# Kernel tuning notes

Hardware: AMD Instinct MI355X
Metric: run time of the kernel (lower is better)

Reference implementation:

```python
import jax, jax.numpy as jnp
import numpy as np

NUM_LAYERS = 25
INPUT = 500
HIDDEN = 64
SEQ = 25
BATCH = 4096
OUT = 10
GATES = 4 * HIDDEN


def setup_inputs() -> dict:
    key = jax.random.key(0)
    ks = jax.random.split(key, 11)
    s = 0.1  # ~ uniform(-1/sqrt(H),1/sqrt(H)) scale used by torch LSTM init
    return {
        "x": jax.random.normal(ks[0], (SEQ, BATCH, INPUT), jnp.float32),
        "W_ih0": jax.random.normal(ks[1], (GATES, INPUT), jnp.float32) * s,
        "W_hh0": jax.random.normal(ks[2], (GATES, HIDDEN), jnp.float32) * s,
        "b_ih0": jax.random.normal(ks[3], (GATES,), jnp.float32) * s,
        "b_hh0": jax.random.normal(ks[4], (GATES,), jnp.float32) * s,
        "W_ih_rest": jax.random.normal(ks[5], (NUM_LAYERS - 1, GATES, HIDDEN), jnp.float32) * s,
        "W_hh_rest": jax.random.normal(ks[6], (NUM_LAYERS - 1, GATES, HIDDEN), jnp.float32) * s,
        "b_ih_rest": jax.random.normal(ks[7], (NUM_LAYERS - 1, GATES), jnp.float32) * s,
        "b_hh_rest": jax.random.normal(ks[8], (NUM_LAYERS - 1, GATES), jnp.float32) * s,
        "W_lin": jax.random.normal(ks[9], (OUT, HIDDEN), jnp.float32) * s,
        "b_lin": jax.random.normal(ks[10], (OUT,), jnp.float32) * s,
    }


def _lstm_layer(seq, Wih, Whh, bih, bhh):
    # seq: [T, B, D_in] -> (outputs [T, B, H], h_T [B, H], c_T [B, H])
    T, B, _ = seq.shape
    H = Whh.shape[1]
    # precompute input projection for all timesteps in one big GEMM
    xp = jnp.einsum('tbi,gi->tbg', seq, Wih) + bih + bhh  # [T, B, 4H]
    h0 = jnp.zeros((B, H), seq.dtype)
    c0 = jnp.zeros((B, H), seq.dtype)

    def step(carry, xpt):
        h, c = carry
        g = xpt + h @ Whh.T  # [B, 4H], torch gate order i, f, g, o
        i, f, gg, o = jnp.split(g, 4, axis=-1)
        c = jax.nn.sigmoid(f) * c + jax.nn.sigmoid(i) * jnp.tanh(gg)
        h = jax.nn.sigmoid(o) * jnp.tanh(c)
        return (h, c), h

    (hT, cT), hs = jax.lax.scan(step, (h0, c0), xp)
    return hs, hT, cT


def reference(x, W_ih0, W_hh0, b_ih0, b_hh0, W_ih_rest, W_hh_rest, b_ih_rest, b_hh_rest, W_lin, b_lin):
    hs, hT, cT = _lstm_layer(x, W_ih0, W_hh0, b_ih0, b_hh0)
    h_list, c_list = [hT], [cT]
    for l in range(NUM_LAYERS - 1):  # fixed small layer count: Python loop ok
        hs, hT, cT = _lstm_layer(hs, W_ih_rest[l], W_hh_rest[l], b_ih_rest[l], b_hh_rest[l])
        h_list.append(hT)
        c_list.append(cT)
    h_n = jnp.stack(h_list)  # [L, B, H]
    c_n = jnp.stack(c_list)  # [L, B, H]
    # faithful to torch: out[:, -1, :] indexes the BATCH dim -> [T, H]
    lstm_out = hs[:, -1, :] @ W_lin.T + b_lin  # [T, OUT]
    return (lstm_out, h_n, c_n)
```

## Files before the change

kernel.cpp:

```cpp
#include <hip/hip_runtime.h>

#define T_SEQ 25
#define NBATCH 4096
#define D_IN 500
#define HID 64
#define NG 256
#define NLAYERS 25
#define NOUT 10

typedef __attribute__((ext_vector_type(8))) short bf16x8;
typedef __attribute__((ext_vector_type(4))) short bf16x4;
typedef __attribute__((ext_vector_type(4))) float f32x4;

#define LOG2E 1.4426950408889634f
#define ROWS 1152
#define RNG_OFF 57600

__device__ __forceinline__ short f2bf(float f) {
    union { float f; unsigned u; } v; v.f = f;
    unsigned u = v.u + 0x7FFFu + ((v.u >> 16) & 1u);
    return (short)(u >> 16);
}
__device__ __forceinline__ float bf2f(short s) {
    union { unsigned u; float f; } v;
    v.u = ((unsigned)(unsigned short)s) << 16;
    return v.f;
}
__device__ __forceinline__ bf16x8 cvt8(f32x4 a, f32x4 b) {
    bf16x8 r;
    r[0]=f2bf(a[0]); r[1]=f2bf(a[1]); r[2]=f2bf(a[2]); r[3]=f2bf(a[3]);
    r[4]=f2bf(b[0]); r[5]=f2bf(b[1]); r[6]=f2bf(b[2]); r[7]=f2bf(b[3]);
    return r;
}

__global__ __launch_bounds__(256)
void prep(const float* __restrict__ Wih0, const float* __restrict__ Whh0,
          const float* __restrict__ WihR, const float* __restrict__ WhhR,
          const float* __restrict__ bihR, const float* __restrict__ bhhR,
          short* __restrict__ wbf2, short* __restrict__ whh0b,
          short* __restrict__ wihRb, short* __restrict__ whhRb,
          float* __restrict__ bsum) {
    int idx = blockIdx.x * 256 + threadIdx.x;
    if (idx < 131072) {
        int j = idx & 7, lane = (idx >> 3) & 63, nt = (idx >> 9) & 15, kc = idx >> 13;
        int n = nt*16 + (lane & 15);
        int k = kc*32 + (lane >> 4)*8 + j;
        wbf2[idx] = (k < D_IN) ? f2bf(Wih0[n * D_IN + k]) : (short)0;
    } else if (idx < 147456) {
        int j = idx - 131072; whh0b[j] = f2bf(Whh0[j]);
    } else if (idx < 540672) {
        int j = idx - 147456; wihRb[j] = f2bf(WihR[j]);
    } else if (idx < 933888) {
        int j = idx - 540672; whhRb[j] = f2bf(WhhR[j]);
    } else if (idx < 940032) {
        int j = idx - 933888; bsum[j] = bihR[j] + bhhR[j];
    }
}

__global__ __launch_bounds__(256, 1)
void xp0_gemm(const float* __restrict__ x, const short* __restrict__ wbf2,
              const float* __restrict__ bih0, const float* __restrict__ bhh0,
              short* __restrict__ xp0b) {
    const int tid = threadIdx.x;
    const int wv = tid >> 6, lane = tid & 63, col = lane & 15, q = lane >> 4;
    const int t  = blockIdx.x >> 5;
    const int b0 = (blockIdx.x & 31) << 7;

    f32x4 acc[2][16];
    #pragma unroll
    for (int nt = 0; nt < 16; nt++) {
        int g = nt*16 + col;
        float bv = bih0[g] + bhh0[g];
        acc[0][nt] = (f32x4){bv,bv,bv,bv};
        acc[1][nt] = acc[0][nt];
    }
    const float* xrow0 = x + ((size_t)t*NBATCH + b0 + wv*32 + col)*D_IN;
    const float* xrow1 = xrow0 + 16*(size_t)D_IN;

    #pragma unroll 3
    for (int kc = 0; kc < 15; kc++) {
        const int ko = kc*32 + q*8;
        const f32x4* p0 = (const f32x4*)(xrow0 + ko);
        const f32x4* p1 = (const f32x4*)(xrow1 + ko);
        bf16x8 a0 = cvt8(p0[0], p0[1]);
        bf16x8 a1 = cvt8(p1[0], p1[1]);
        #pragma unroll
        for (int nt = 0; nt < 16; nt++) {
            bf16x8 bfr = *(const bf16x8*)(wbf2 + ((size_t)(kc*16+nt)*64 + lane)*8);
            acc[0][nt] = __builtin_amdgcn_mfma_f32_16x16x32_bf16(a0, bfr, acc[0][nt], 0,0,0);
            acc[1][nt] = __builtin_amdgcn_mfma_f32_16x16x32_bf16(a1, bfr, acc[1][nt], 0,0,0);
        }
    }
    {
        f32x4 z = (f32x4){0.f,0.f,0.f,0.f};
        f32x4 lo0=z, hi0=z, lo1=z, hi1=z;
        const int ko = 480 + q*8;
        if (q < 2) {
            lo0 = *(const f32x4*)(xrow0 + ko); hi0 = *(const f32x4*)(xrow0 + ko + 4);
            lo1 = *(const f32x4*)(xrow1 + ko); hi1 = *(const f32x4*)(xrow1 + ko + 4);
        } else if (q == 2) {
            lo0 = *(const f32x4*)(xrow0 + 496);
            lo1 = *(const f32x4*)(xrow1 + 496);
        }
        bf16x8 a0 = cvt8(lo0, hi0);
        bf16x8 a1 = cvt8(lo1, hi1);
        #pragma unroll
        for (int nt = 0; nt < 16; nt++) {
            bf16x8 bfr = *(const bf16x8*)(wbf2 + ((size_t)(15*16+nt)*64 + lane)*8);
            acc[0][nt] = __builtin_amdgcn_mfma_f32_16x16x32_bf16(a0, bfr, acc[0][nt], 0,0,0);
            acc[1][nt] = __builtin_amdgcn_mfma_f32_16x16x32_bf16(a1, bfr, acc[1][nt], 0,0,0);
        }
    }
    #pragma unroll
    for (int ms = 0; ms < 2; ms++) {
        #pragma unroll
        for (int nt = 0; nt < 16; nt++) {
            int g = nt*16 + col;
            int b = b0 + wv*32 + ms*16 + q*4;
            bf16x4 o;
            o[0]=f2bf(acc[ms][nt][0]); o[1]=f2bf(acc[ms][nt][1]);
            o[2]=f2bf(acc[ms][nt][2]); o[3]=f2bf(acc[ms][nt][3]);
            *(bf16x4*)(xp0b + ((size_t)t*NG + g)*NBATCH + b) = o;
        }
    }
}


#define GATES(ACC, OUTB, LAYER, TT)                                            \
    do {                                                                       \
        _Pragma("unroll")                                                      \
        for (int rr = 0; rr < 4; rr++) {                                       \
            float iv = ACC[0][rr], fv = ACC[1][rr];                            \
            float gv = ACC[2][rr], ov = ACC[3][rr];                            \
            float gc = fminf(fmaxf(gv, -30.f), 30.f);                          \
            float ei = __builtin_amdgcn_exp2f(-LOG2E * iv);                    \
            float eg = __builtin_amdgcn_exp2f((2.f*LOG2E) * gc);               \
            float ef = __builtin_amdgcn_exp2f(-LOG2E * fv);                    \
            float it = (eg - 1.f) *                                            \
                __builtin_amdgcn_rcpf((1.f + ei) * (1.f + eg));                \
            float cn = __builtin_amdgcn_rcpf(1.f + ef) * c4[rr] + it;          \
            c4[rr] = cn;                                                       \
            float cc = fminf(fmaxf(cn, -30.f), 30.f);                          \
            float eo = __builtin_amdgcn_exp2f(-LOG2E * ov);                    \
            float ec = __builtin_amdgcn_exp2f((2.f*LOG2E) * cc);               \
            float hn = (ec - 1.f) *                                            \
                __builtin_amdgcn_rcpf((1.f + eo) * (1.f + ec));                \
            lds[(OUTB) + (q*4+rr)*72 + hh] = f2bf(hn);                         \
            if ((TT) == 24) {                                                  \
                size_t oi = ((size_t)(LAYER)*NBATCH + b0 + q*4 + rr)*HID + hh; \
                h_n[oi] = hn; c_n[oi] = cn;                                    \
            }                                                                  \
        }                                                                      \
    } while (0)

__global__ __launch_bounds__(512, 1)
void lstm_persist(const short* __restrict__ whh0b, const short* __restrict__ wihRb,
                  const short* __restrict__ whhRb, const float* __restrict__ bsum,
                  const float* __restrict__ Wlin, const float* __restrict__ blin,
                  const short* __restrict__ xp0b, float* __restrict__ out) {
    __shared__ short lds[2*T_SEQ*ROWS + 4*ROWS];
    const int tid = threadIdx.x;
    const int wv = tid >> 6, lane = tid & 63, col = lane & 15, q = lane >> 4;
    const int grp = wv >> 2;
    const int hh  = (wv & 3)*16 + col;
    const int b0  = blockIdx.x << 4;
    float* __restrict__ h_n = out + 250;
    float* __restrict__ c_n = out + 250 + (size_t)NLAYERS*NBATCH*HID;

    int pOff = T_SEQ*ROWS, oOff = 0;
    bf16x8 wih[4][2], whh[4][2];
    float bias[4];
    float c4[4] = {0.f,0.f,0.f,0.f};

    bf16x4 xpn[4];
    if (grp == 0) {
        #pragma unroll
        for (int gt = 0; gt < 4; gt++) {
            const short* wr = whh0b + (size_t)(gt*64 + hh)*64;
            whh[gt][0] = *(const bf16x8*)(wr + q*8);
            whh[gt][1] = *(const bf16x8*)(wr + 32 + q*8);
            xpn[gt] = *(const bf16x4*)(xp0b + ((size_t)(gt*64 + hh))*NBATCH + b0 + q*4);
        }
    }
    for (int t = 0; t < T_SEQ; t++) {
        if (grp == 0) {
            f32x4 acc[4];
            #pragma unroll
            for (int gt = 0; gt < 4; gt++) {
                f32x4 p;
                p[0]=bf2f(xpn[gt][0]); p[1]=bf2f(xpn[gt][1]);
                p[2]=bf2f(xpn[gt][2]); p[3]=bf2f(xpn[gt][3]);
                acc[gt] = p;
            }
            if (t < T_SEQ-1) {
                #pragma unroll
                for (int gt = 0; gt < 4; gt++)
                    xpn[gt] = *(const bf16x4*)(xp0b + (((size_t)(t+1))*NG + gt*64 + hh)*NBATCH + b0 + q*4);
            }
            if (t > 0) {
                const int rb = oOff + (t-1)*ROWS + col*72;
                bf16x8 h0 = *(const bf16x8*)&lds[rb + q*8];
                bf16x8 h1 = *(const bf16x8*)&lds[rb + 32 + q*8];
                #pragma unroll
                for (int gt = 0; gt < 4; gt++) {
                    acc[gt] = __builtin_amdgcn_mfma_f32_16x16x32_bf16(h0, whh[gt][0], acc[gt], 0,0,0);
                    acc[gt] = __builtin_amdgcn_mfma_f32_16x16x32_bf16(h1, whh[gt][1], acc[gt], 0,0,0);
                }
            }
            const int ob = oOff + t*ROWS;
            GATES(acc, ob, 0, t);
        }
        __syncthreads();
    }

    #pragma unroll 1
    for (int r = 0; r < 12; r++) {
        { int tm = pOff; pOff = oOff; oOff = tm; }
        const int myl = grp ? (2*r + 2) : (2*r + 1);
        const short* wi = wihRb + (size_t)(myl-1)*16384;
        const short* wh = whhRb + (size_t)(myl-1)*16384;
        #pragma unroll
        for (int gt = 0; gt < 4; gt++) {
            int g = gt*64 + hh;
            wih[gt][0] = *(const bf16x8*)(wi + (size_t)g*64 + q*8);
            wih[gt][1] = *(const bf16x8*)(wi + (size_t)g*64 + 32 + q*8);
            whh[gt][0] = *(const bf16x8*)(wh + (size_t)g*64 + q*8);
            whh[gt][1] = *(const bf16x8*)(wh + (size_t)g*64 + 32 + q*8);
            bias[gt] = bsum[(size_t)(myl-1)*NG + g];
        }
        c4[0]=c4[1]=c4[2]=c4[3]=0.f;

        #pragma unroll 1
        for (int s = 0; s < 26; s++) {
            const int t = s - grp;
            if (t >= 0 && t < T_SEQ) {
                const int in_base  = grp ? (RNG_OFF + (t&3)*ROWS) : (pOff + t*ROWS);
                const int out_base = grp ? (oOff + t*ROWS)        : (RNG_OFF + (t&3)*ROWS);
                f32x4 acc[4];
                #pragma unroll
                for (int gt = 0; gt < 4; gt++)
                    acc[gt] = (f32x4){bias[gt],bias[gt],bias[gt],bias[gt]};
                {
                    const int ib = in_base + col*72;
                    bf16x8 a0 = *(const bf16x8*)&lds[ib + q*8];
                    bf16x8 a1 = *(const bf16x8*)&lds[ib + 32 + q*8];
                    #pragma unroll
                    for (int gt = 0; gt < 4; gt++) {
                        acc[gt] = __builtin_amdgcn_mfma_f32_16x16x32_bf16(a0, wih[gt][0], acc[gt], 0,0,0);
                        acc[gt] = __builtin_amdgcn_mfma_f32_16x16x32_bf16(a1, wih[gt][1], acc[gt], 0,0,0);
                    }
                }
                if (t > 0) {
                    const int rb = (grp ? (oOff + (t-1)*ROWS) : (RNG_OFF + ((t-1)&3)*ROWS)) + col*72;
                    bf16x8 h0 = *(const bf16x8*)&lds[rb + q*8];
                    bf16x8 h1 = *(const bf16x8*)&lds[rb + 32 + q*8];
                    #pragma unroll
                    for (int gt = 0; gt < 4; gt++) {
                        acc[gt] = __builtin_amdgcn_mfma_f32_16x16x32_bf16(h0, whh[gt][0], acc[gt], 0,0,0);
                        acc[gt] = __builtin_amdgcn_mfma_f32_16x16x32_bf16(h1, whh[gt][1], acc[gt], 0,0,0);
                    }
                }
                GATES(acc, out_base, myl, t);
            }
            __syncthreads();
        }
    }

    if (blockIdx.x == 255 && tid < T_SEQ*NOUT) {
        int ti = tid / NOUT, o = tid - ti*NOUT;
        float s = blin[o];
        #pragma unroll
        for (int k = 0; k < HID; k++)
            s += bf2f(lds[oOff + ti*ROWS + 15*72 + k]) * Wlin[o*HID + k];
        out[tid] = s;
    }
}

extern "C" void kernel_launch(void* const* d_in, const int* in_sizes, int n_in,
                              void* d_out, int out_size, void* d_ws, size_t ws_size,
                              hipStream_t stream) {
    const float* x    = (const float*)d_in[0];
    const float* Wih0 = (const float*)d_in[1];
    const float* Whh0 = (const float*)d_in[2];
    const float* bih0 = (const float*)d_in[3];
    const float* bhh0 = (const float*)d_in[4];
    const float* WihR = (const float*)d_in[5];
    const float* WhhR = (const float*)d_in[6];
    const float* bihR = (const float*)d_in[7];
    const float* bhhR = (const float*)d_in[8];
    const float* Wlin = (const float*)d_in[9];
    const float* blin = (const float*)d_in[10];
    float* out = (float*)d_out;

    short* xp0b  = (short*)d_ws;
    short* wbf2  = xp0b  + 26214400;
    short* whh0b = wbf2  + 131072;
    short* wihRb = whh0b + 16384;
    short* whhRb = wihRb + 393216;
    float* bsum  = (float*)(whhRb + 393216);

    prep<<<dim3(3672), dim3(256), 0, stream>>>(Wih0, Whh0, WihR, WhhR, bihR, bhhR,
                                               wbf2, whh0b, wihRb, whhRb, bsum);
    xp0_gemm<<<dim3(800), dim3(256), 0, stream>>>(x, wbf2, bih0, bhh0, xp0b);
    lstm_persist<<<dim3(NBATCH/16), dim3(512), 0, stream>>>(
        whh0b, wihRb, whhRb, bsum, Wlin, blin, xp0b, out);
}
```

Baseline: 718.5 us.

## Pipeline LSTM layers across four waves, each computing full gate tile

The persistent LSTM kernel now runs 256 threads, and each of four waves owns a whole layer, holding all 16 gate tiles in registers. Layers are pipelined in a wavefront: wave w runs layer 4*pass+w, offset by one timestep, and passes hidden states through small LDS ring buffers, with a full-sequence wrap buffer linking wave 3 back to wave 0. This replaces the previous two-group scheme, which paired layers and split gates across waves, and is meant to raise layer-level parallelism and cut the number of barrier steps (181 steps versus about 337). In exchange, each wave carries much higher register pressure (32 weight fragments per matrix plus 16 accumulators) and does more serial MFMA work per step, and the final linear now reads fp32 h values saved in a separate buffer.

```diff
diff --git a/kernel.cpp b/kernel.cpp
--- a/kernel.cpp
+++ b/kernel.cpp
@@ -13,8 +13,11 @@
 typedef __attribute__((ext_vector_type(4))) float f32x4;
 
 #define LOG2E 1.4426950408889634f
-#define ROWS 1152
-#define RNG_OFF 57600
+
+#define SLOT 1152
+#define RING_STRIDE (4*SLOT)
+#define WRAP_OFF (3*RING_STRIDE)
+#define LDS_SHORTS (WRAP_OFF + 26*SLOT)
 
 __device__ __forceinline__ short f2bf(float f) {
     union { float f; unsigned u; } v; v.f = f;
@@ -125,154 +128,154 @@
     }
 }
 
-
-#define GATES(ACC, OUTB, LAYER, TT)                                            \
-    do {                                                                       \
-        _Pragma("unroll")                                                      \
-        for (int rr = 0; rr < 4; rr++) {                                       \
-            float iv = ACC[0][rr], fv = ACC[1][rr];                            \
-            float gv = ACC[2][rr], ov = ACC[3][rr];                            \
-            float gc = fminf(fmaxf(gv, -30.f), 30.f);                          \
-            float ei = __builtin_amdgcn_exp2f(-LOG2E * iv);                    \
-            float eg = __builtin_amdgcn_exp2f((2.f*LOG2E) * gc);               \
-            float ef = __builtin_amdgcn_exp2f(-LOG2E * fv);                    \
-            float it = (eg - 1.f) *                                            \
-                __builtin_amdgcn_rcpf((1.f + ei) * (1.f + eg));                \
-            float cn = __builtin_amdgcn_rcpf(1.f + ef) * c4[rr] + it;          \
-            c4[rr] = cn;                                                       \
-            float cc = fminf(fmaxf(cn, -30.f), 30.f);                          \
-            float eo = __builtin_amdgcn_exp2f(-LOG2E * ov);                    \
-            float ec = __builtin_amdgcn_exp2f((2.f*LOG2E) * cc);               \
-            float hn = (ec - 1.f) *                                            \
-                __builtin_amdgcn_rcpf((1.f + eo) * (1.f + ec));                \
-            lds[(OUTB) + (q*4+rr)*72 + hh] = f2bf(hn);                         \
-            if ((TT) == 24) {                                                  \
-                size_t oi = ((size_t)(LAYER)*NBATCH + b0 + q*4 + rr)*HID + hh; \
-                h_n[oi] = hn; c_n[oi] = cn;                                    \
-            }                                                                  \
-        }                                                                      \
-    } while (0)
-
-__global__ __launch_bounds__(512, 1)
+__global__ __launch_bounds__(256, 1)
 void lstm_persist(const short* __restrict__ whh0b, const short* __restrict__ wihRb,
                   const short* __restrict__ whhRb, const float* __restrict__ bsum,
                   const float* __restrict__ Wlin, const float* __restrict__ blin,
                   const short* __restrict__ xp0b, float* __restrict__ out) {
-    __shared__ short lds[2*T_SEQ*ROWS + 4*ROWS];
+    __shared__ short lds[LDS_SHORTS];
+    __shared__ float h24[T_SEQ*HID];
     const int tid = threadIdx.x;
-    const int wv = tid >> 6, lane = tid & 63, col = lane & 15, q = lane >> 4;
-    const int grp = wv >> 2;
-    const int hh  = (wv & 3)*16 + col;
-    const int b0  = blockIdx.x << 4;
+    const int w = tid >> 6, lane = tid & 63, col = lane & 15, q = lane >> 4;
+    const int b0 = blockIdx.x << 4;
     float* __restrict__ h_n = out + 250;
-    float* __restrict__ c_n = out + 250 + (size_t)NLAYERS*NBATCH*HID;
-
-    int pOff = T_SEQ*ROWS, oOff = 0;
-    bf16x8 wih[4][2], whh[4][2];
-    float bias[4];
-    float c4[4] = {0.f,0.f,0.f,0.f};
-
-    bf16x4 xpn[4];
-    if (grp == 0) {
-        #pragma unroll
-        for (int gt = 0; gt < 4; gt++) {
-            const short* wr = whh0b + (size_t)(gt*64 + hh)*64;
-            whh[gt][0] = *(const bf16x8*)(wr + q*8);
-            whh[gt][1] = *(const bf16x8*)(wr + 32 + q*8);
-            xpn[gt] = *(const bf16x4*)(xp0b + ((size_t)(gt*64 + hh))*NBATCH + b0 + q*4);
-        }
-    }
-    for (int t = 0; t < T_SEQ; t++) {
-        if (grp == 0) {
-            f32x4 acc[4];
-            #pragma unroll
-            for (int gt = 0; gt < 4; gt++) {
-                f32x4 p;
-                p[0]=bf2f(xpn[gt][0]); p[1]=bf2f(xpn[gt][1]);
-                p[2]=bf2f(xpn[gt][2]); p[3]=bf2f(xpn[gt][3]);
-                acc[gt] = p;
-            }
-            if (t < T_SEQ-1) {
-                #pragma unroll
-                for (int gt = 0; gt < 4; gt++)
-                    xpn[gt] = *(const bf16x4*)(xp0b + (((size_t)(t+1))*NG + gt*64 + hh)*NBATCH + b0 + q*4);
+    float* __restrict__ c_n = h_n + (size_t)NLAYERS*NBATCH*HID;
+
+    bf16x8 wih[16][2], whh[16][2];
+    float bias[16];
+    float c16[16];
+    bf16x4 xpn[16];
+
+    if (w == 0) {
+        #pragma unroll
+        for (int nt = 0; nt < 16; nt++) {
+            const short* wr = whh0b + (nt*16 + col)*64;
+            whh[nt][0] = *(const bf16x8*)(wr + q*8);
+            whh[nt][1] = *(const bf16x8*)(wr + 32 + q*8);
+            bias[nt] = 0.f;
+            xpn[nt] = *(const bf16x4*)(xp0b + (size_t)(nt*16 + col)*NBATCH + b0 + q*4);
+        }
+    } else {
+        const short* wi = wihRb + (w-1)*16384;
+        const short* wh = whhRb + (w-1)*16384;
+        #pragma unroll
+        for (int nt = 0; nt < 16; nt++) {
+            int g = nt*16 + col;
+            wih[nt][0] = *(const bf16x8*)(wi + g*64 + q*8);
+            wih[nt][1] = *(const bf16x8*)(wi + g*64 + 32 + q*8);
+            whh[nt][0] = *(const bf16x8*)(wh + g*64 + q*8);
+            whh[nt][1] = *(const bf16x8*)(wh + g*64 + 32 + q*8);
+            bias[nt] = bsum[(w-1)*NG + g];
+        }
+    }
+    #pragma unroll
+    for (int i = 0; i < 16; i++) c16[i] = 0.f;
+
+    int pass = 0, tt = -w;
+    #pragma unroll 1
+    for (int s = 0; s < 181; s++) {
+        const int l = 4*pass + w;
+        if (tt >= 0 && tt < 25 && l <= (w == 0 ? 24 : 23)) {
+            const int t = tt;
+            f32x4 acc[16];
+            if (l == 0) {
+                #pragma unroll
+                for (int nt = 0; nt < 16; nt++) {
+                    f32x4 p;
+                    p[0]=bf2f(xpn[nt][0]); p[1]=bf2f(xpn[nt][1]);
+                    p[2]=bf2f(xpn[nt][2]); p[3]=bf2f(xpn[nt][3]);
+                    acc[nt] = p;
+                }
+                if (t < 24) {
+                    #pragma unroll
+                    for (int nt = 0; nt < 16; nt++)
+                        xpn[nt] = *(const bf16x4*)(xp0b +
+                            ((size_t)(t+1)*NG + nt*16 + col)*NBATCH + b0 + q*4);
+                }
+            } else {
+                #pragma unroll
+                for (int nt = 0; nt < 16; nt++)
+                    acc[nt] = (f32x4){bias[nt],bias[nt],bias[nt],bias[nt]};
+                const int inb = (w == 0 ? WRAP_OFF + t*SLOT
+                                        : (w-1)*RING_STRIDE + (t&3)*SLOT) + col*72;
+                bf16x8 a0 = *(const bf16x8*)&lds[inb + q*8];
+                bf16x8 a1 = *(const bf16x8*)&lds[inb + 32 + q*8];
+                #pragma unroll
+                for (int nt = 0; nt < 16; nt++) {
+                    acc[nt] = __builtin_amdgcn_mfma_f32_16x16x32_bf16(a0, wih[nt][0], acc[nt], 0,0,0);
+                    acc[nt] = __builtin_amdgcn_mfma_f32_16x16x32_bf16(a1, wih[nt][1], acc[nt], 0,0,0);
+                }
             }
             if (t > 0) {
-                const int rb = oOff + (t-1)*ROWS + col*72;
+                const int rb = (w == 3 ? WRAP_OFF + (t-1)*SLOT
+                                       : w*RING_STRIDE + ((t-1)&3)*SLOT) + col*72;
                 bf16x8 h0 = *(const bf16x8*)&lds[rb + q*8];
                 bf16x8 h1 = *(const bf16x8*)&lds[rb + 32 + q*8];
                 #pragma unroll
-                for (int gt = 0; gt < 4; gt++) {
-                    acc[gt] = __builtin_amdgcn_mfma_f32_16x16x32_bf16(h0, whh[gt][0], acc[gt], 0,0,0);
-                    acc[gt] = __builtin_amdgcn_mfma_f32_16x16x32_bf16(h1, whh[gt][1], acc[gt], 0,0,0);
+                for (int nt = 0; nt < 16; nt++) {
+                    acc[nt] = __builtin_amdgcn_mfma_f32_16x16x32_bf16(h0, whh[nt][0], acc[nt], 0,0,0);
+                    acc[nt] = __builtin_amdgcn_mfma_f32_16x16x32_bf16(h1, whh[nt][1], acc[nt], 0,0,0);
                 }
             }
-            const int ob = oOff + t*ROWS;
-            GATES(acc, ob, 0, t);
+            const int ob = (w == 3 ? WRAP_OFF + t*SLOT : w*RING_STRIDE + (t&3)*SLOT);
+            #pragma unroll
+            for (int hg = 0; hg < 4; hg++) {
+                #pragma unroll
+                for (int rr = 0; rr < 4; rr++) {
+                    float iv = acc[hg][rr],    fv = acc[4+hg][rr];
+                    float gv = acc[8+hg][rr],  ov = acc[12+hg][rr];
+                    float gc = fminf(fmaxf(gv, -30.f), 30.f);
+                    float ei = __builtin_amdgcn_exp2f(-LOG2E * iv);
+                    float eg = __builtin_amdgcn_exp2f((2.f*LOG2E) * gc);
+                    float ef = __builtin_amdgcn_exp2f(-LOG2E * fv);
+                    float it = (eg - 1.f) *
+                        __builtin_amdgcn_rcpf((1.f + ei) * (1.f + eg));
+                    float cn = __builtin_amdgcn_rcpf(1.f + ef) * c16[hg*4+rr] + it;
+                    c16[hg*4+rr] = cn;
+                    float cc = fminf(fmaxf(cn, -30.f), 30.f);
+                    float eo = __builtin_amdgcn_exp2f(-LOG2E * ov);
+                    float ec = __builtin_amdgcn_exp2f((2.f*LOG2E) * cc);
+                    float hn = (ec - 1.f) *
+                        __builtin_amdgcn_rcpf((1.f + eo) * (1.f + ec));
+                    lds[ob + (q*4+rr)*72 + hg*16 + col] = f2bf(hn);
+                    if (t == 24) {
+                        size_t oi = ((size_t)l*NBATCH + b0 + q*4 + rr)*HID + hg*16 + col;
+                        h_n[oi] = hn; c_n[oi] = cn;
+                    }
+                    if (l == 24 && q == 3 && rr == 3)
+                        h24[t*HID + hg*16 + col] = hn;
+                }
+            }
+        } else if (tt == 25) {
+            int nl = 4*(pass+1) + w;
+            if (nl <= (w == 0 ? 24 : 23)) {
+                const short* wi = wihRb + (size_t)(nl-1)*16384;
+                const short* wh = whhRb + (size_t)(nl-1)*16384;
+                #pragma unroll
+                for (int nt = 0; nt < 16; nt++) {
+                    int g = nt*16 + col;
+                    wih[nt][0] = *(const bf16x8*)(wi + g*64 + q*8);
+                    wih[nt][1] = *(const bf16x8*)(wi + g*64 + 32 + q*8);
+                    whh[nt][0] = *(const bf16x8*)(wh + g*64 + q*8);
+                    whh[nt][1] = *(const bf16x8*)(wh + g*64 + 32 + q*8);
+                    bias[nt] = bsum[(size_t)(nl-1)*NG + g];
+                }
+            }
+            #pragma unroll
+            for (int i = 0; i < 16; i++) c16[i] = 0.f;
         }
         __syncthreads();
-    }
-
-    #pragma unroll 1
-    for (int r = 0; r < 12; r++) {
-        { int tm = pOff; pOff = oOff; oOff = tm; }
-        const int myl = grp ? (2*r + 2) : (2*r + 1);
-        const short* wi = wihRb + (size_t)(myl-1)*16384;
-        const short* wh = whhRb + (size_t)(myl-1)*16384;
-        #pragma unroll
-        for (int gt = 0; gt < 4; gt++) {
-            int g = gt*64 + hh;
-            wih[gt][0] = *(const bf16x8*)(wi + (size_t)g*64 + q*8);
-            wih[gt][1] = *(const bf16x8*)(wi + (size_t)g*64 + 32 + q*8);
-            whh[gt][0] = *(const bf16x8*)(wh + (size_t)g*64 + q*8);
-            whh[gt][1] = *(const bf16x8*)(wh + (size_t)g*64 + 32 + q*8);
-            bias[gt] = bsum[(size_t)(myl-1)*NG + g];
-        }
-        c4[0]=c4[1]=c4[2]=c4[3]=0.f;
-
-        #pragma unroll 1
-        for (int s = 0; s < 26; s++) {
-            const int t = s - grp;
-            if (t >= 0 && t < T_SEQ) {
-                const int in_base  = grp ? (RNG_OFF + (t&3)*ROWS) : (pOff + t*ROWS);
-                const int out_base = grp ? (oOff + t*ROWS)        : (RNG_OFF + (t&3)*ROWS);
-                f32x4 acc[4];
-                #pragma unroll
-                for (int gt = 0; gt < 4; gt++)
-                    acc[gt] = (f32x4){bias[gt],bias[gt],bias[gt],bias[gt]};
-                {
-                    const int ib = in_base + col*72;
-                    bf16x8 a0 = *(const bf16x8*)&lds[ib + q*8];
-                    bf16x8 a1 = *(const bf16x8*)&lds[ib + 32 + q*8];
-                    #pragma unroll
-                    for (int gt = 0; gt < 4; gt++) {
-                        acc[gt] = __builtin_amdgcn_mfma_f32_16x16x32_bf16(a0, wih[gt][0], acc[gt], 0,0,0);
-                        acc[gt] = __builtin_amdgcn_mfma_f32_16x16x32_bf16(a1, wih[gt][1], acc[gt], 0,0,0);
-                    }
-                }
-                if (t > 0) {
-                    const int rb = (grp ? (oOff + (t-1)*ROWS) : (RNG_OFF + ((t-1)&3)*ROWS)) + col*72;
-                    bf16x8 h0 = *(const bf16x8*)&lds[rb + q*8];
-                    bf16x8 h1 = *(const bf16x8*)&lds[rb + 32 + q*8];
-                    #pragma unroll
-                    for (int gt = 0; gt < 4; gt++) {
-                        acc[gt] = __builtin_amdgcn_mfma_f32_16x16x32_bf16(h0, whh[gt][0], acc[gt], 0,0,0);
-                        acc[gt] = __builtin_amdgcn_mfma_f32_16x16x32_bf16(h1, whh[gt][1], acc[gt], 0,0,0);
-                    }
-                }
-                GATES(acc, out_base, myl, t);
-            }
-            __syncthreads();
-        }
+        tt++;
+        if (tt == 26) { tt = 0; pass++; }
     }
 
     if (blockIdx.x == 255 && tid < T_SEQ*NOUT) {
         int ti = tid / NOUT, o = tid - ti*NOUT;
-        float s = blin[o];
+        float sacc = blin[o];
         #pragma unroll
         for (int k = 0; k < HID; k++)
-            s += bf2f(lds[oOff + ti*ROWS + 15*72 + k]) * Wlin[o*HID + k];
-        out[tid] = s;
+            sacc += h24[ti*HID + k] * Wlin[o*HID + k];
+        out[tid] = sacc;
     }
 }
 
@@ -302,6 +305,6 @@
     prep<<<dim3(3672), dim3(256), 0, stream>>>(Wih0, Whh0, WihR, WhhR, bihR, bhhR,
                                                wbf2, whh0b, wihRb, whhRb, bsum);
     xp0_gemm<<<dim3(800), dim3(256), 0, stream>>>(x, wbf2, bih0, bhh0, xp0b);
-    lstm_persist<<<dim3(NBATCH/16), dim3(512), 0, stream>>>(
+    lstm_persist<<<dim3(NBATCH/16), dim3(256), 0, stream>>>(
         whh0b, wihRb, whhRb, bsum, Wlin, blin, xp0b, out);
 }
```

After: 1.540 ms. 2.14x slower.
